# Performance work log

Hardware: AMD Instinct MI355X
Metric: run time of the kernel (lower is better)

## Reference

```python
import jax, jax.numpy as jnp
import numpy as np

EMBED = 512  # scale uses embed_size**-0.5 per the original forward (NOT head_size)


def setup_inputs() -> dict:
    key = jax.random.key(0)
    k1, k2, k3, k4 = jax.random.split(key, 4)
    B, T, D, H = 8, 4096, EMBED, 64
    inputs = jax.random.normal(k1, (B, T, D), dtype=jnp.float32)
    Wq = jax.random.normal(k2, (D, H), dtype=jnp.float32) * (D ** -0.5)
    Wk = jax.random.normal(k3, (D, H), dtype=jnp.float32) * (D ** -0.5)
    Wv = jax.random.normal(k4, (D, H), dtype=jnp.float32) * (D ** -0.5)
    return {"inputs": inputs, "Wq": Wq, "Wk": Wk, "Wv": Wv}


def reference(inputs, Wq, Wk, Wv):
    # inputs: [B, T, D]; Wq/Wk/Wv: [D, H]
    B, T, D = inputs.shape
    q = inputs @ Wq  # [B, T, H]
    k = inputs @ Wk  # [B, T, H]
    v = inputs @ Wv  # [B, T, H]
    scale = jnp.asarray(D, inputs.dtype) ** -0.5  # original scales by embed_size**-0.5
    scores = jnp.einsum('bth,bsh->bts', q, k) * scale  # [B, T, T]
    causal = jnp.arange(T)[:, None] >= jnp.arange(T)[None, :]  # lower-triangular
    scores = jnp.where(causal, scores, jnp.asarray(-jnp.inf, scores.dtype))
    weights = jax.nn.softmax(scores, axis=-1)
    # dropout is identity in eval mode
    return weights @ v  # [B, T, H]
```

## Files before the change

kernel.cpp:

```cpp
#include <hip/hip_runtime.h>
#include <hip/hip_bf16.h>
#include <math.h>

#define TSEQ 4096
#define NB 8
#define DEM 512
#define HD 64
#define KP 66
#define VP 34
#define WIP 136
#define WIMG 26624
#define QSZ ((size_t)NB * TSEQ * HD)
#define SLOTS_PER_B 144

typedef __attribute__((ext_vector_type(8))) short short8;
typedef __attribute__((ext_vector_type(4))) short short4v;
typedef __attribute__((ext_vector_type(4))) float float4v;
typedef __attribute__((ext_vector_type(16))) float f32x16;

__device__ __forceinline__ short f2bf(float f) {
    union { float f; unsigned u; } v; v.f = f;
    unsigned r = v.u + 0x7fffu + ((v.u >> 16) & 1u);
    return (short)(r >> 16);
}

__device__ __forceinline__ short8 pack8(float4 a, float4 b) {
    union { short8 s; __hip_bfloat162 h[4]; } u;
    u.h[0] = __float22bfloat162_rn(make_float2(a.x, a.y));
    u.h[1] = __float22bfloat162_rn(make_float2(a.z, a.w));
    u.h[2] = __float22bfloat162_rn(make_float2(b.x, b.y));
    u.h[3] = __float22bfloat162_rn(make_float2(b.z, b.w));
    return u.s;
}

__device__ __forceinline__ int pkbf2(float x, float y) {
    union { __hip_bfloat162 h; int i; } u;
    u.h = __float22bfloat162_rn(make_float2(x, y));
    return u.i;
}

__device__ __forceinline__ short8 mk8(int a, int b, int c, int d) {
    union { short8 s; int i[4]; } u;
    u.i[0] = a; u.i[1] = b; u.i[2] = c; u.i[3] = d;
    return u.s;
}

__device__ __forceinline__ void gload_lds16(const void* g, void* l) {
    __builtin_amdgcn_global_load_lds(
        (const __attribute__((address_space(1))) unsigned int*)g,
        (__attribute__((address_space(3))) unsigned int*)l,
        16, 0, 0);
}

__device__ __host__ __forceinline__ int slot_base(int mq) {
    int a = mq >> 2, r = mq & 3;
    return (a + 1) * (2 * a + r);
}

__global__ __launch_bounds__(256) void wtr_kernel(
    const float* __restrict__ Wq, const float* __restrict__ Wk,
    const float* __restrict__ Wv, short* __restrict__ wimg)
{
    __shared__ float t[64][65];
    const int tid = threadIdx.x;
    const int kb = blockIdx.x;
    const int k0 = kb * 64;
    const int m = blockIdx.y;
    const int c = kb >> 1, half = kb & 1;
    const float* W = (m == 0) ? Wq : ((m == 1) ? Wk : Wv);
    const float sc = (m == 0) ? 0.044194173824159216f : 1.0f;

#pragma unroll
    for (int i = 0; i < 4; ++i) {
        int f = tid + 256 * i;
        int k = f >> 4, n4 = (f & 15) * 4;
        float4 wv = *(const float4*)&W[(k0 + k) * HD + n4];
        t[k][n4 + 0] = wv.x; t[k][n4 + 1] = wv.y;
        t[k][n4 + 2] = wv.z; t[k][n4 + 3] = wv.w;
    }
    __syncthreads();
#pragma unroll
    for (int i = 0; i < 4; ++i) {
        int f = tid + 256 * i;
        int n = f >> 4, k4 = (f & 15) * 4;
        short4v o;
        o[0] = f2bf(t[k4 + 0][n] * sc);
        o[1] = f2bf(t[k4 + 1][n] * sc);
        o[2] = f2bf(t[k4 + 2][n] * sc);
        o[3] = f2bf(t[k4 + 3][n] * sc);
        *(short4v*)&wimg[c * WIMG + (64 * m + n) * WIP + half * 64 + k4] = o;
    }
}

__global__ __launch_bounds__(256, 2) void qkv_mfma(
    const float* __restrict__ x, const short* __restrict__ wimg,
    short* __restrict__ q, short* __restrict__ k, short* __restrict__ vt)
{
    __shared__ alignas(16) short wlds[WIMG];

    const int tid = threadIdx.x;
    const int w = tid >> 6;
    const int l15 = tid & 15;
    const int quad = (tid >> 4) & 3;
    const int rbase = blockIdx.x * 64 + w * 16 + l15;

    const float* xr = x + (size_t)rbase * DEM;
    float4v acc[12] = {};

    for (int c = 0; c < 4; ++c) {
        __syncthreads();
        {
            const char* gsrc = (const char*)(wimg + c * WIMG) + tid * 16;
            char* ldst = (char*)wlds + tid * 16;
#pragma unroll
            for (int i = 0; i < 13; ++i)
                gload_lds16(gsrc + i * 4096, ldst + i * 4096);
        }
        __syncthreads();

#pragma unroll
        for (int ks = 0; ks < 4; ++ks) {
            const int k0 = c * 128 + ks * 32 + quad * 8;
            float4 xa = *(const float4*)&xr[k0];
            float4 xb = *(const float4*)&xr[k0 + 4];
            short8 xv = pack8(xa, xb);
            const int lk = ks * 32 + quad * 8;
#pragma unroll
            for (int mt = 0; mt < 12; ++mt) {
                short8 wf = *(const short8*)&wlds[(mt * 16 + l15) * WIP + lk];
                acc[mt] = __builtin_amdgcn_mfma_f32_16x16x32_bf16(wf, xv, acc[mt], 0, 0, 0);
            }
        }
    }

#pragma unroll
    for (int mt = 0; mt < 8; ++mt) {
        short* dst = (mt < 4) ? q : k;
        short4v o;
        o[0] = f2bf(acc[mt][0]); o[1] = f2bf(acc[mt][1]);
        o[2] = f2bf(acc[mt][2]); o[3] = f2bf(acc[mt][3]);
        *(short4v*)&dst[(size_t)rbase * HD + (mt & 3) * 16 + quad * 4] = o;
    }
    const int b = rbase >> 12, t = rbase & (TSEQ - 1);
#pragma unroll
    for (int mt = 8; mt < 12; ++mt) {
#pragma unroll
        for (int reg = 0; reg < 4; ++reg) {
            int d = (mt - 8) * 16 + quad * 4 + reg;
            vt[((size_t)(b * HD + d)) * TSEQ + t] = f2bf(acc[mt][reg]);
        }
    }
}

__global__ __launch_bounds__(64, 3) void flash_mfma(
    const short* __restrict__ qw, const short* __restrict__ kw,
    const short* __restrict__ vtw, float* __restrict__ out,
    float* __restrict__ pO, float* __restrict__ stS)
{
    __shared__ short kt[32 * KP];
    __shared__ short vl[64 * VP];

    const int lane = threadIdx.x;
    const int q5 = lane & 31;
    const int hi = lane >> 5;
    const int bx = blockIdx.x;
    const int b = bx & 7;
    const int r = bx >> 3;
    const int w = r & 3;
    const int idx = r >> 2;

    int mq, j;
    if (idx < 120) {
        int t = idx;
        mq = 31; j = 0;
#pragma unroll 1
        for (int mm = 31; mm >= 3; --mm) {
            int f = (mm + 1) >> 2;
            if (t < f) { mq = mm; j = t; break; }
            t -= f;
        }
    } else {
        int t = idx - 120;
        int kc = t >> 3, p = t & 7;
        mq = (30 - kc) - 4 * p;
        j = (mq + 1) >> 2;
    }
    const int r0 = mq * 128;
    const int ss0 = 16 * j;
    const int ssend = min(16 * (j + 1), 4 * mq + w + 1);
    const int slot = b * SLOTS_PER_B + slot_base(mq) + j;
    const int qrow = r0 + w * 32 + q5;

    short8 qf[4];
    {
        const short* qp = qw + ((size_t)(b * TSEQ + qrow)) * HD + hi * 8;
#pragma unroll
        for (int ks = 0; ks < 4; ++ks) qf[ks] = *(const short8*)(qp + ks * 16);
    }

    f32x16 O0 = {}, O1 = {};
    float l_lane = 0.f;

    const short* kbase = kw + (size_t)b * TSEQ * HD;
    const short* vbase = vtw + (size_t)b * HD * TSEQ;
    const int krow = lane >> 3, kc8 = (lane & 7) * 8;
    const int vrow = lane >> 2, vc8 = (lane & 3) * 8;

    short8 pk0, pk1, pk2, pk3, pv0, pv1, pv2, pv3;
    {
        const short* kg = kbase + (size_t)(ss0 * 32) * HD;
        const short* vg = vbase + ss0 * 32;
        pk0 = *(const short8*)(kg + (krow +  0) * HD + kc8);
        pk1 = *(const short8*)(kg + (krow +  8) * HD + kc8);
        pk2 = *(const short8*)(kg + (krow + 16) * HD + kc8);
        pk3 = *(const short8*)(kg + (krow + 24) * HD + kc8);
        pv0 = *(const short8*)(vg + (size_t)(vrow +  0) * TSEQ + vc8);
        pv1 = *(const short8*)(vg + (size_t)(vrow + 16) * TSEQ + vc8);
        pv2 = *(const short8*)(vg + (size_t)(vrow + 32) * TSEQ + vc8);
        pv3 = *(const short8*)(vg + (size_t)(vrow + 48) * TSEQ + vc8);
    }

    for (int ss = ss0; ss < ssend; ++ss) {
        __syncthreads();
        *(short8*)&kt[(krow +  0) * KP + kc8] = pk0;
        *(short8*)&kt[(krow +  8) * KP + kc8] = pk1;
        *(short8*)&kt[(krow + 16) * KP + kc8] = pk2;
        *(short8*)&kt[(krow + 24) * KP + kc8] = pk3;
        *(short8*)&vl[(vrow +  0) * VP + vc8] = pv0;
        *(short8*)&vl[(vrow + 16) * VP + vc8] = pv1;
        *(short8*)&vl[(vrow + 32) * VP + vc8] = pv2;
        *(short8*)&vl[(vrow + 48) * VP + vc8] = pv3;
        __syncthreads();

        if (ss + 1 < ssend) {
            const short* kg = kbase + (size_t)((ss + 1) * 32) * HD;
            const short* vg = vbase + (ss + 1) * 32;
            pk0 = *(const short8*)(kg + (krow +  0) * HD + kc8);
            pk1 = *(const short8*)(kg + (krow +  8) * HD + kc8);
            pk2 = *(const short8*)(kg + (krow + 16) * HD + kc8);
            pk3 = *(const short8*)(kg + (krow + 24) * HD + kc8);
            pv0 = *(const short8*)(vg + (size_t)(vrow +  0) * TSEQ + vc8);
            pv1 = *(const short8*)(vg + (size_t)(vrow + 16) * TSEQ + vc8);
            pv2 = *(const short8*)(vg + (size_t)(vrow + 32) * TSEQ + vc8);
            pv3 = *(const short8*)(vg + (size_t)(vrow + 48) * TSEQ + vc8);
        }

        f32x16 S = {};
#pragma unroll
        for (int ks = 0; ks < 4; ++ks) {
            short8 a = *(const short8*)&kt[q5 * KP + ks * 16 + hi * 8];
            S = __builtin_amdgcn_mfma_f32_32x32x16_bf16(a, qf[ks], S, 0, 0, 0);
        }

        if (ss * 32 + 31 > r0 + w * 32) {
#pragma unroll
            for (int reg = 0; reg < 16; ++reg) {
                int key = ss * 32 + (reg & 3) + 8 * (reg >> 2) + 4 * hi;
                if (key > qrow) S[reg] = -INFINITY;
            }
        }

        float p[16];
#pragma unroll
        for (int reg = 0; reg < 16; ++reg) {
            p[reg] = __expf(S[reg]);
            l_lane += p[reg];
        }
        int dd[4][2];
#pragma unroll
        for (int a = 0; a < 4; ++a) {
            dd[a][0] = pkbf2(p[4 * a + 0], p[4 * a + 1]);
            dd[a][1] = pkbf2(p[4 * a + 2], p[4 * a + 3]);
        }
        int ra0 = __shfl_xor(hi ? dd[0][0] : dd[1][0], 32, 64);
        int ra1 = __shfl_xor(hi ? dd[0][1] : dd[1][1], 32, 64);
        int rb0 = __shfl_xor(hi ? dd[2][0] : dd[3][0], 32, 64);
        int rb1 = __shfl_xor(hi ? dd[2][1] : dd[3][1], 32, 64);
        short8 PA0 = hi ? mk8(ra0, ra1, dd[1][0], dd[1][1])
                        : mk8(dd[0][0], dd[0][1], ra0, ra1);
        short8 PA1 = hi ? mk8(rb0, rb1, dd[3][0], dd[3][1])
                        : mk8(dd[2][0], dd[2][1], rb0, rb1);

#pragma unroll
        for (int kr = 0; kr < 2; ++kr) {
            short8 pa = kr ? PA1 : PA0;
            short8 v0 = *(const short8*)&vl[(q5)      * VP + kr * 16 + hi * 8];
            short8 v1 = *(const short8*)&vl[(32 + q5) * VP + kr * 16 + hi * 8];
            O0 = __builtin_amdgcn_mfma_f32_32x32x16_bf16(pa, v0, O0, 0, 0, 0);
            O1 = __builtin_amdgcn_mfma_f32_32x32x16_bf16(pa, v1, O1, 0, 0, 0);
        }
    }

    const float ltot = l_lane + __shfl_xor(l_lane, 32, 64);

    if (mq <= 3) {
        float inv = 1.0f / ltot;
#pragma unroll
        for (int reg = 0; reg < 16; ++reg) {
            int qloc = (reg & 3) + 8 * (reg >> 2) + 4 * hi;
            float ir = __shfl(inv, qloc, 64);
            size_t rowb = (size_t)(b * TSEQ + r0 + w * 32 + qloc) * HD + q5;
            out[rowb]      = O0[reg] * ir;
            out[rowb + 32] = O1[reg] * ir;
        }
    } else {
        float* dest = pO + ((size_t)slot * 128 + w * 32) * HD + q5;
#pragma unroll
        for (int reg = 0; reg < 16; ++reg) {
            int qloc = (reg & 3) + 8 * (reg >> 2) + 4 * hi;
            dest[(size_t)qloc * HD]      = O0[reg];
            dest[(size_t)qloc * HD + 32] = O1[reg];
        }
        if (hi == 0) stS[slot * 128 + w * 32 + q5] = ltot;
    }
}

__global__ __launch_bounds__(256) void merge_kernel(
    float* __restrict__ out, const float* __restrict__ pO,
    const float* __restrict__ stS)
{
    const int tid = threadIdx.x;
    const int bx = blockIdx.x;
    const int b = bx / 56, loc = bx - b * 56;
    const int t = 512 + loc * 64 + (tid >> 2);
    const int dq = (tid & 3) * 16;
    const int mq = t >> 7, rr = t & 127;
    const int nseg = (mq + 4) >> 2;
    const int sb = b * SLOTS_PER_B + slot_base(mq);

    float denom = 0.f;
    for (int s = 0; s < nseg; ++s) denom += stS[(sb + s) * 128 + rr];
    float inv = 1.0f / denom;

    float4 o[4] = {};
    for (int s = 0; s < nseg; ++s) {
        const float4* pp = (const float4*)
            &pO[((size_t)(sb + s) * 128 + rr) * HD + dq];
#pragma unroll
        for (int i = 0; i < 4; ++i) {
            float4 p = pp[i];
            o[i].x += p.x; o[i].y += p.y;
            o[i].z += p.z; o[i].w += p.w;
        }
    }
    float4* op = (float4*)&out[((size_t)b * TSEQ + t) * HD + dq];
#pragma unroll
    for (int i = 0; i < 4; ++i) {
        o[i].x *= inv; o[i].y *= inv; o[i].z *= inv; o[i].w *= inv;
        op[i] = o[i];
    }
}

extern "C" void kernel_launch(void* const* d_in, const int* in_sizes, int n_in,
                              void* d_out, int out_size, void* d_ws, size_t ws_size,
                              hipStream_t stream) {
    const float* x  = (const float*)d_in[0];
    const float* Wq = (const float*)d_in[1];
    const float* Wk = (const float*)d_in[2];
    const float* Wv = (const float*)d_in[3];
    float* out = (float*)d_out;

    short* q  = (short*)d_ws;
    short* k  = q + QSZ;
    short* vt = k + QSZ;
    short* wimg = vt + QSZ;
    float* pO = (float*)(wimg + 4 * WIMG);
    float* stS = pO + (size_t)NB * SLOTS_PER_B * 128 * HD;

    wtr_kernel<<<dim3(8, 3), 256, 0, stream>>>(Wq, Wk, Wv, wimg);
    qkv_mfma<<<dim3(NB * TSEQ / 64), 256, 0, stream>>>(x, wimg, q, k, vt);
    flash_mfma<<<dim3(NB * SLOTS_PER_B * 4), 64, 0, stream>>>(q, k, vt, out, pO, stS);
    merge_kernel<<<dim3(448), 256, 0, stream>>>(out, pO, stS);
}
```

Before: 157.7 us.

## Prefetch x in QKV GEMM, pack two waves per flash block, use exp2

The QKV projection now prefetches the next chunk of x rows into registers before the MFMA loop, so global loads overlap with compute. The flash kernel packs two independent waves per 128-thread block, each with its own LDS K/V buffers, removes the now-unnecessary __syncthreads, and raises MFMA priority with s_setprio. QK^T is split into two independent accumulators to shorten the dependency chain. The scale folds log2(e) into Wq so softmax can use hardware exp2. Together these cut barrier, latency and transcendental cost, but add register and LDS pressure and change the occupancy hint.

Measured after the change: 251.8 us. 1.6x slower.

```diff
diff --git a/kernel.cpp b/kernel.cpp
--- a/kernel.cpp
+++ b/kernel.cpp
@@ -68,7 +68,8 @@
     const int m = blockIdx.y;
     const int c = kb >> 1, half = kb & 1;
     const float* W = (m == 0) ? Wq : ((m == 1) ? Wk : Wv);
-    const float sc = (m == 0) ? 0.044194173824159216f : 1.0f;
+    const float sc = (m == 0) ? (0.044194173824159216f * 1.4426950408889634f)
+                              : 1.0f;
 
 #pragma unroll
     for (int i = 0; i < 4; ++i) {
@@ -107,6 +108,13 @@
     const float* xr = x + (size_t)rbase * DEM;
     float4v acc[12] = {};
 
+    float4 xa[4], xb[4];
+#pragma unroll
+    for (int ks = 0; ks < 4; ++ks) {
+        xa[ks] = *(const float4*)&xr[ks * 32 + quad * 8];
+        xb[ks] = *(const float4*)&xr[ks * 32 + quad * 8 + 4];
+    }
+
     for (int c = 0; c < 4; ++c) {
         __syncthreads();
         {
@@ -116,19 +124,26 @@
             for (int i = 0; i < 13; ++i)
                 gload_lds16(gsrc + i * 4096, ldst + i * 4096);
         }
+        short8 xv[4];
+#pragma unroll
+        for (int ks = 0; ks < 4; ++ks) xv[ks] = pack8(xa[ks], xb[ks]);
         __syncthreads();
 
+        if (c + 1 < 4) {
+#pragma unroll
+            for (int ks = 0; ks < 4; ++ks) {
+                xa[ks] = *(const float4*)&xr[(c + 1) * 128 + ks * 32 + quad * 8];
+                xb[ks] = *(const float4*)&xr[(c + 1) * 128 + ks * 32 + quad * 8 + 4];
+            }
+        }
+
 #pragma unroll
         for (int ks = 0; ks < 4; ++ks) {
-            const int k0 = c * 128 + ks * 32 + quad * 8;
-            float4 xa = *(const float4*)&xr[k0];
-            float4 xb = *(const float4*)&xr[k0 + 4];
-            short8 xv = pack8(xa, xb);
             const int lk = ks * 32 + quad * 8;
 #pragma unroll
             for (int mt = 0; mt < 12; ++mt) {
                 short8 wf = *(const short8*)&wlds[(mt * 16 + l15) * WIP + lk];
-                acc[mt] = __builtin_amdgcn_mfma_f32_16x16x32_bf16(wf, xv, acc[mt], 0, 0, 0);
+                acc[mt] = __builtin_amdgcn_mfma_f32_16x16x32_bf16(wf, xv[ks], acc[mt], 0, 0, 0);
             }
         }
     }
@@ -152,22 +167,24 @@
     }
 }
 
-__global__ __launch_bounds__(64, 3) void flash_mfma(
+__global__ __launch_bounds__(128, 4) void flash_mfma(
     const short* __restrict__ qw, const short* __restrict__ kw,
     const short* __restrict__ vtw, float* __restrict__ out,
     float* __restrict__ pO, float* __restrict__ stS)
 {
-    __shared__ short kt[32 * KP];
-    __shared__ short vl[64 * VP];
-
-    const int lane = threadIdx.x;
+    __shared__ short kt[2][32 * KP];
+    __shared__ short vl[2][64 * VP];
+
+    const int tid = threadIdx.x;
+    const int wv = tid >> 6;
+    const int lane = tid & 63;
     const int q5 = lane & 31;
     const int hi = lane >> 5;
     const int bx = blockIdx.x;
     const int b = bx & 7;
-    const int r = bx >> 3;
-    const int w = r & 3;
-    const int idx = r >> 2;
+    const int rr = bx >> 3;
+    const int wp = rr & 1;
+    const int idx = rr >> 1;
 
     int mq, j;
     if (idx < 120) {
@@ -185,6 +202,7 @@
         mq = (30 - kc) - 4 * p;
         j = (mq + 1) >> 2;
     }
+    const int w = 2 * wp + wv;
     const int r0 = mq * 128;
     const int ss0 = 16 * j;
     const int ssend = min(16 * (j + 1), 4 * mq + w + 1);
@@ -205,6 +223,8 @@
     const short* vbase = vtw + (size_t)b * HD * TSEQ;
     const int krow = lane >> 3, kc8 = (lane & 7) * 8;
     const int vrow = lane >> 2, vc8 = (lane & 3) * 8;
+    short* ktw = kt[wv];
+    short* vlw = vl[wv];
 
     short8 pk0, pk1, pk2, pk3, pv0, pv1, pv2, pv3;
     {
@@ -221,16 +241,14 @@
     }
 
     for (int ss = ss0; ss < ssend; ++ss) {
-        __syncthreads();
-        *(short8*)&kt[(krow +  0) * KP + kc8] = pk0;
-        *(short8*)&kt[(krow +  8) * KP + kc8] = pk1;
-        *(short8*)&kt[(krow + 16) * KP + kc8] = pk2;
-        *(short8*)&kt[(krow + 24) * KP + kc8] = pk3;
-        *(short8*)&vl[(vrow +  0) * VP + vc8] = pv0;
-        *(short8*)&vl[(vrow + 16) * VP + vc8] = pv1;
-        *(short8*)&vl[(vrow + 32) * VP + vc8] = pv2;
-        *(short8*)&vl[(vrow + 48) * VP + vc8] = pv3;
-        __syncthreads();
+        *(short8*)&ktw[(krow +  0) * KP + kc8] = pk0;
+        *(short8*)&ktw[(krow +  8) * KP + kc8] = pk1;
+        *(short8*)&ktw[(krow + 16) * KP + kc8] = pk2;
+        *(short8*)&ktw[(krow + 24) * KP + kc8] = pk3;
+        *(short8*)&vlw[(vrow +  0) * VP + vc8] = pv0;
+        *(short8*)&vlw[(vrow + 16) * VP + vc8] = pv1;
+        *(short8*)&vlw[(vrow + 32) * VP + vc8] = pv2;
+        *(short8*)&vlw[(vrow + 48) * VP + vc8] = pv3;
 
         if (ss + 1 < ssend) {
             const short* kg = kbase + (size_t)((ss + 1) * 32) * HD;
@@ -245,12 +263,20 @@
             pv3 = *(const short8*)(vg + (size_t)(vrow + 48) * TSEQ + vc8);
         }
 
-        f32x16 S = {};
-#pragma unroll
-        for (int ks = 0; ks < 4; ++ks) {
-            short8 a = *(const short8*)&kt[q5 * KP + ks * 16 + hi * 8];
-            S = __builtin_amdgcn_mfma_f32_32x32x16_bf16(a, qf[ks], S, 0, 0, 0);
-        }
+        f32x16 Sa = {}, Sb = {};
+        __builtin_amdgcn_s_setprio(1);
+        {
+            short8 a0 = *(const short8*)&ktw[q5 * KP +  0 + hi * 8];
+            short8 a1 = *(const short8*)&ktw[q5 * KP + 16 + hi * 8];
+            short8 a2 = *(const short8*)&ktw[q5 * KP + 32 + hi * 8];
+            short8 a3 = *(const short8*)&ktw[q5 * KP + 48 + hi * 8];
+            Sa = __builtin_amdgcn_mfma_f32_32x32x16_bf16(a0, qf[0], Sa, 0, 0, 0);
+            Sb = __builtin_amdgcn_mfma_f32_32x32x16_bf16(a2, qf[2], Sb, 0, 0, 0);
+            Sa = __builtin_amdgcn_mfma_f32_32x32x16_bf16(a1, qf[1], Sa, 0, 0, 0);
+            Sb = __builtin_amdgcn_mfma_f32_32x32x16_bf16(a3, qf[3], Sb, 0, 0, 0);
+        }
+        __builtin_amdgcn_s_setprio(0);
+        f32x16 S = Sa + Sb;
 
         if (ss * 32 + 31 > r0 + w * 32) {
 #pragma unroll
@@ -263,7 +289,7 @@
         float p[16];
 #pragma unroll
         for (int reg = 0; reg < 16; ++reg) {
-            p[reg] = __expf(S[reg]);
+            p[reg] = __builtin_amdgcn_exp2f(S[reg]);
             l_lane += p[reg];
         }
         int dd[4][2];
@@ -281,14 +307,16 @@
         short8 PA1 = hi ? mk8(rb0, rb1, dd[3][0], dd[3][1])
                         : mk8(dd[2][0], dd[2][1], rb0, rb1);
 
+        __builtin_amdgcn_s_setprio(1);
 #pragma unroll
         for (int kr = 0; kr < 2; ++kr) {
             short8 pa = kr ? PA1 : PA0;
-            short8 v0 = *(const short8*)&vl[(q5)      * VP + kr * 16 + hi * 8];
-            short8 v1 = *(const short8*)&vl[(32 + q5) * VP + kr * 16 + hi * 8];
+            short8 v0 = *(const short8*)&vlw[(q5)      * VP + kr * 16 + hi * 8];
+            short8 v1 = *(const short8*)&vlw[(32 + q5) * VP + kr * 16 + hi * 8];
             O0 = __builtin_amdgcn_mfma_f32_32x32x16_bf16(pa, v0, O0, 0, 0, 0);
             O1 = __builtin_amdgcn_mfma_f32_32x32x16_bf16(pa, v1, O1, 0, 0, 0);
         }
+        __builtin_amdgcn_s_setprio(0);
     }
 
     const float ltot = l_lane + __shfl_xor(l_lane, 32, 64);
@@ -369,6 +397,6 @@
 
     wtr_kernel<<<dim3(8, 3), 256, 0, stream>>>(Wq, Wk, Wv, wimg);
     qkv_mfma<<<dim3(NB * TSEQ / 64), 256, 0, stream>>>(x, wimg, q, k, vt);
-    flash_mfma<<<dim3(NB * SLOTS_PER_B * 4), 64, 0, stream>>>(q, k, vt, out, pO, stS);
+    flash_mfma<<<dim3(NB * SLOTS_PER_B * 2), 128, 0, stream>>>(q, k, vt, out, pO, stS);
     merge_kernel<<<dim3(448), 256, 0, stream>>>(out, pO, stS);
 }
```
